# Kernel optimization log

Measured on AMD Instinct MI355X. Metric: run time of the kernel, lower is better.

## Reference

```python
import jax, jax.numpy as jnp
import numpy as np

N = 8192
INPUT_DIM = 256
HIDDEN_DIM = 16
K_NEIGHBORS = 6


def setup_inputs() -> dict:
    key = jax.random.key(0)
    k1, k2 = jax.random.split(key)
    x = jax.random.normal(k1, (N, INPUT_DIM), dtype=jnp.float32)
    W = jax.random.normal(k2, (HIDDEN_DIM, INPUT_DIM), dtype=jnp.float32) * (1.0 / np.sqrt(INPUT_DIM))
    b = jnp.zeros((HIDDEN_DIM,), dtype=jnp.float32)
    return {"x": x, "W": W, "b": b}


def reference(x, W, b):
    num_nodes = x.shape[0]
    # Linear projection then L2-normalize rows (F.normalize, p=2, dim=1, eps=1e-12)
    h = x @ W.T + b                                   # [N, H]
    norm = jnp.linalg.norm(h, axis=1, keepdims=True)
    h = h / jnp.maximum(norm, 1e-12)
    sim = h @ h.T                                     # [N, N] cosine similarity
    k = min(K_NEIGHBORS, num_nodes - 1)
    # top-(k+1) per row; drop the first (self, sim=1 is the max)
    top_vals, top_idx = jax.lax.top_k(sim, k + 1)     # [N, k+1]
    neigh_idx = top_idx[:, 1:]                        # [N, k]
    neigh_vals = top_vals[:, 1:]                      # [N, k]
    rows = jnp.arange(num_nodes)[:, None]             # [N, 1]
    adj = jnp.zeros_like(sim).at[rows, neigh_idx].set(neigh_vals)
    adj = (adj + adj.T) * 0.5
    row_sums = adj.sum(axis=1, keepdims=True)
    adj = adj / (row_sums + 1e-8)
    return adj
```

## Files before the change

kernel.cpp:

```cpp
#include <hip/hip_runtime.h>
#include <stdint.h>
#include <math.h>

#define NN   8192
#define IND  256
#define HID  16
#define KN   6
#define SEG  8
#define SW   (NN/SEG)
#define CCOL 256
#define NCH  (SW/CCOL)
#define TPC  (CCOL/16)


typedef short s8v  __attribute__((ext_vector_type(8)));
typedef float f4v  __attribute__((ext_vector_type(4)));

__device__ __forceinline__ uint32_t fflip(float f) {
    const uint32_t u = __float_as_uint(f);
    return (u & 0x80000000u) ? ~u : (u | 0x80000000u);
}

__device__ __forceinline__ uint32_t bf16_rne_bits(float x) {
    const uint32_t u = __float_as_uint(x);
    return (u + 0x7FFFu + ((u >> 16) & 1u)) & 0xFFFF0000u;
}

__global__ __launch_bounds__(256) void k1_embed(const float* __restrict__ x,
                                                const float* __restrict__ W,
                                                const float* __restrict__ b,
                                                ushort* __restrict__ PA1,
                                                ushort* __restrict__ PA2,
                                                ushort* __restrict__ PA3,
                                                ushort* __restrict__ PB1,
                                                ushort* __restrict__ PB2,
                                                float* __restrict__ rs,
                                                int* __restrict__ cnt)
{
    const int lane = threadIdx.x & 63;
    const int wv   = threadIdx.x >> 6;
    const int row  = blockIdx.x * 4 + wv;

    const float4 xv = *(const float4*)(x + (size_t)row * IND + lane * 4);

    float hv[HID];
#pragma unroll
    for (int k = 0; k < HID; ++k) {
        const float4 wv4 = *(const float4*)(W + (size_t)k * IND + lane * 4);
        float v = xv.x * wv4.x + xv.y * wv4.y + xv.z * wv4.z + xv.w * wv4.w;
#pragma unroll
        for (int m = 32; m >= 1; m >>= 1) v += __shfl_xor(v, m, 64);
        hv[k] = v;
    }

    float ss = 0.f;
#pragma unroll
    for (int k = 0; k < HID; ++k) { hv[k] = hv[k] + b[k]; ss += hv[k] * hv[k]; }
    const float nrm = fmaxf(sqrtf(ss), 1e-12f);
#pragma unroll
    for (int k = 0; k < HID; ++k) hv[k] = hv[k] / nrm;

    if (lane == 0) { rs[row] = 0.f; cnt[row] = 0; }

    if (lane < 32) {
        const int s = lane, k = s & 15;
        const float xx = hv[k];
        const uint32_t hb = bf16_rne_bits(xx);
        const float r1 = xx - __uint_as_float(hb);
        const uint32_t mb = bf16_rne_bits(r1);
        const float r2 = r1 - __uint_as_float(mb);
        const uint32_t lb = bf16_rne_bits(r2);
        const ushort hi = (ushort)(hb >> 16);
        const ushort mi = (ushort)(mb >> 16);
        const ushort lo = (ushort)(lb >> 16);

        const bool f = (s < 16);
        const size_t t = (size_t)row * 32 + s;
        PA1[t] = hi;
        PA2[t] = f ? mi : hi;
        PA3[t] = f ? lo : mi;
        PB1[t] = f ? hi : mi;
        PB2[t] = f ? hi : lo;
    }
}

#define CSWPF(X,i,j) { const float _h = fmaxf(X[i], X[j]); const float _l = fminf(X[i], X[j]); X[i] = _h; X[j] = _l; }
#define CSWPV(a,b)   { const float _h = fmaxf(a, b); const float _l = fminf(a, b); a = _h; b = _l; }
#define BSTAGES(X) CSWPF(X,0,4) CSWPF(X,1,5) CSWPF(X,2,6) CSWPF(X,3,7) \
                   CSWPF(X,0,2) CSWPF(X,1,3) CSWPF(X,4,6) CSWPF(X,5,7) \
                   CSWPF(X,0,1) CSWPF(X,2,3) CSWPF(X,4,5) CSWPF(X,6,7)

__global__ __launch_bounds__(256, 4) void p1_scan(const ushort* __restrict__ PA1,
                                                  const ushort* __restrict__ PA2,
                                                  const ushort* __restrict__ PA3,
                                                  const ushort* __restrict__ PB1,
                                                  const ushort* __restrict__ PB2,
                                                  float* __restrict__ tq)
{
    __shared__ s8v lds[2048];

    const int tid  = threadIdx.x;
    const int lane = tid & 63;
    const int wv   = tid >> 6;
    const int seg  = blockIdx.x & (SEG - 1);
    const int row0 = (blockIdx.x >> 3) * 64 + wv * 16;
    const int n    = lane & 15;
    const int q    = lane >> 4;
    const int qs   = (q + ((n >> 1) & 3)) & 3;

    const size_t ioff = ((size_t)(row0 + n) << 5) + (q << 3);
    const s8v i1 = *(const s8v*)(PA1 + ioff);
    const s8v i2 = *(const s8v*)(PA2 + ioff);
    const s8v i3 = *(const s8v*)(PA3 + ioff);

    float L[8];
#pragma unroll
    for (int t = 0; t < 8; ++t) L[t] = -INFINITY;

    for (int cc = 0; cc < NCH; ++cc) {
        __syncthreads();
#pragma unroll
        for (int it = 0; it < 8; ++it) {
            const int o  = it * 256 + tid;
            const int oo = o & 1023;
            const int c  = oo >> 2;
            const int qq = oo & 3;
            const int sw = (qq + ((c >> 1) & 3)) & 3;
            const ushort* src = (it < 4) ? PB1 : PB2;
            const int gcol = seg * SW + cc * CCOL + c;
            const s8v v = *(const s8v*)(src + ((size_t)gcol << 5) + (qq << 3));
            lds[((it < 4) ? 0 : 1024) + (c << 2) + sw] = v;
        }
        __syncthreads();

        const int base = (n << 2) + qs;
#pragma unroll 4
        for (int t = 0; t < TPC; ++t) {
            const s8v jb1 = lds[t * 64 + base];
            const s8v jb2 = lds[1024 + t * 64 + base];

            f4v acc = {0.f, 0.f, 0.f, 0.f};
            acc = __builtin_amdgcn_mfma_f32_16x16x32_bf16(jb1, i1, acc, 0, 0, 0);
            acc = __builtin_amdgcn_mfma_f32_16x16x32_bf16(jb2, i2, acc, 0, 0, 0);
            acc = __builtin_amdgcn_mfma_f32_16x16x32_bf16(jb1, i3, acc, 0, 0, 0);

            float s0 = acc[0], s1 = acc[1], s2 = acc[2], s3 = acc[3];
            CSWPV(s0, s1) CSWPV(s2, s3) CSWPV(s0, s2) CSWPV(s1, s3) CSWPV(s1, s2)

            L[4] = fmaxf(L[4], s3);
            L[5] = fmaxf(L[5], s2);
            L[6] = fmaxf(L[6], s1);
            L[7] = fmaxf(L[7], s0);
            BSTAGES(L)
        }
    }

#pragma unroll
    for (int mm = 16; mm <= 32; mm <<= 1) {
        float o[8], X[8];
#pragma unroll
        for (int t = 0; t < 8; ++t) o[t] = __shfl_xor(L[t], mm, 64);
#pragma unroll
        for (int t = 0; t < 8; ++t) X[t] = fmaxf(L[t], o[7 - t]);
        BSTAGES(X)
#pragma unroll
        for (int t = 0; t < 8; ++t) L[t] = X[t];
    }

    if (q == 0) {
        float* dst = tq + ((size_t)seg * NN + (row0 + n)) * 8;
#pragma unroll
        for (int t = 0; t < 8; ++t) dst[t] = L[t];
    }
}

__global__ __launch_bounds__(256, 4) void p2_emit(const ushort* __restrict__ PA1,
                                                  const ushort* __restrict__ PA2,
                                                  const ushort* __restrict__ PA3,
                                                  const ushort* __restrict__ PB1,
                                                  const ushort* __restrict__ PB2,
                                                  const float* __restrict__ tq,
                                                  int* __restrict__ cnt,
                                                  float* __restrict__ candv,
                                                  int* __restrict__ candj)
{
    __shared__ s8v lds[2048];
    __shared__ float tau_s[64];

    const int tid  = threadIdx.x;
    const int lane = tid & 63;
    const int wv   = tid >> 6;
    const int seg  = blockIdx.x & (SEG - 1);
    const int rg0  = (blockIdx.x >> 3) * 64;
    const int row0 = rg0 + wv * 16;
    const int n    = lane & 15;
    const int q    = lane >> 4;
    const int qs   = (q + ((n >> 1) & 3)) & 3;
    const int row  = row0 + n;

    if (tid < 64) {
        const int r = rg0 + tid;
        float hd[SEG]; int ix[SEG];
#pragma unroll
        for (int s = 0; s < SEG; ++s) { hd[s] = tq[((size_t)s * NN + r) * 8]; ix[s] = 0; }
        float tv0 = -INFINITY;
#pragma unroll
        for (int t = 0; t < 8; ++t) {
            float best = hd[0]; int bs = 0;
#pragma unroll
            for (int s = 1; s < SEG; ++s)
                if (hd[s] > best) { best = hd[s]; bs = s; }
            tv0 = best;
            ++ix[bs];
            hd[bs] = (ix[bs] < 8) ? tq[((size_t)bs * NN + r) * 8 + ix[bs]] : -INFINITY;
        }
        tau_s[tid] = tv0;
    }
    __syncthreads();
    const float tv = tau_s[wv * 16 + n];

    const size_t ioff = ((size_t)row << 5) + (q << 3);
    const s8v i1 = *(const s8v*)(PA1 + ioff);
    const s8v i2 = *(const s8v*)(PA2 + ioff);
    const s8v i3 = *(const s8v*)(PA3 + ioff);

    for (int cc = 0; cc < NCH; ++cc) {
        __syncthreads();
#pragma unroll
        for (int it = 0; it < 8; ++it) {
            const int o  = it * 256 + tid;
            const int oo = o & 1023;
            const int c  = oo >> 2;
            const int qq = oo & 3;
            const int sw = (qq + ((c >> 1) & 3)) & 3;
            const ushort* src = (it < 4) ? PB1 : PB2;
            const int gcol = seg * SW + cc * CCOL + c;
            const s8v v = *(const s8v*)(src + ((size_t)gcol << 5) + (qq << 3));
            lds[((it < 4) ? 0 : 1024) + (c << 2) + sw] = v;
        }
        __syncthreads();

        const int base = (n << 2) + qs;
#pragma unroll 4
        for (int t = 0; t < TPC; ++t) {
            const s8v jb1 = lds[t * 64 + base];
            const s8v jb2 = lds[1024 + t * 64 + base];

            f4v acc = {0.f, 0.f, 0.f, 0.f};
            acc = __builtin_amdgcn_mfma_f32_16x16x32_bf16(jb1, i1, acc, 0, 0, 0);
            acc = __builtin_amdgcn_mfma_f32_16x16x32_bf16(jb2, i2, acc, 0, 0, 0);
            acc = __builtin_amdgcn_mfma_f32_16x16x32_bf16(jb1, i3, acc, 0, 0, 0);

            const float vm = fmaxf(fmaxf(acc[0], acc[1]), fmaxf(acc[2], acc[3]));
            if (__builtin_expect(vm >= tv, 0)) {
                const int jbase = seg * SW + cc * CCOL + t * 16 + (q << 2);
#pragma unroll
                for (int g = 0; g < 4; ++g) {
                    if (acc[g] >= tv) {
                        const int idx = atomicAdd(&cnt[row], 1);
                        if (idx < 16) {
                            candv[(size_t)row * 16 + idx] = acc[g];
                            candj[(size_t)row * 16 + idx] = jbase + g;
                        }
                    }
                }
            }
        }
    }
}

__global__ __launch_bounds__(256) void p3_select(const int* __restrict__ cnt,
                                                 const float* __restrict__ candv,
                                                 const int* __restrict__ candj,
                                                 int* __restrict__ nbr_idx,
                                                 float* __restrict__ nbr_val,
                                                 float* __restrict__ rs)
{
    const int row = blockIdx.x * 256 + threadIdx.x;
    const int c = min(cnt[row], 16);
    uint64_t keys[16];
    for (int i = 0; i < c; ++i) {
        const float v = candv[(size_t)row * 16 + i];
        const uint32_t j = (uint32_t)candj[(size_t)row * 16 + i];
        keys[i] = ((uint64_t)fflip(v) << 32) | (uint64_t)(~j);
    }
    for (int t = 0; t < 7; ++t) {
        uint64_t best = 0; int bi = 0;
        for (int i = 0; i < c; ++i)
            if (keys[i] > best) { best = keys[i]; bi = i; }
        keys[bi] = 0;
        if (t >= 1) {
            uint32_t u = (uint32_t)(best >> 32);
            u = (u & 0x80000000u) ? (u & 0x7fffffffu) : ~u;
            const float v = __uint_as_float(u);
            const int j = (int)~(uint32_t)best;
            nbr_val[(size_t)row * KN + (t - 1)] = v;
            nbr_idx[(size_t)row * KN + (t - 1)] = j;
            atomicAdd(&rs[row], v * 0.5f);
            atomicAdd(&rs[j],   v * 0.5f);
        }
    }
}

__global__ __launch_bounds__(256) void k5_scatter(const int* __restrict__ nbr_idx,
                                                  const float* __restrict__ nbr_val,
                                                  const float* __restrict__ rs,
                                                  float* __restrict__ out)
{
    const int e = blockIdx.x * 256 + threadIdx.x;
    const int i = e / KN;
    const int j = nbr_idx[e];
    const float v = nbr_val[e] * 0.5f;
    const float wi = v / (rs[i] + 1e-8f);
    const float wj = v / (rs[j] + 1e-8f);
    atomicAdd(out + (size_t)i * NN + j, wi);
    atomicAdd(out + (size_t)j * NN + i, wj);
}

extern "C" void kernel_launch(void* const* d_in, const int* in_sizes, int n_in,
                              void* d_out, int out_size, void* d_ws, size_t ws_size,
                              hipStream_t stream)
{
    const float* x = (const float*)d_in[0];
    const float* W = (const float*)d_in[1];
    const float* b = (const float*)d_in[2];
    float* out = (float*)d_out;

    float* tq    = (float*)d_ws;
    float* rs    = tq + (size_t)SEG * NN * 8;
    float* nv    = rs + NN;
    float* candv = nv + (size_t)NN * KN;
    int*   ni    = (int*)(candv + (size_t)NN * 16);
    int*   candj = ni + (size_t)NN * KN;
    int*   cnt   = candj + (size_t)NN * 16;
    ushort* PA1  = (ushort*)(cnt + NN);
    ushort* PA2  = PA1 + (size_t)NN * 32;
    ushort* PA3  = PA2 + (size_t)NN * 32;
    ushort* PB1  = PA3 + (size_t)NN * 32;
    ushort* PB2  = PB1 + (size_t)NN * 32;

    k1_embed <<<NN / 4,            256, 0, stream>>>(x, W, b, PA1, PA2, PA3, PB1, PB2, rs, cnt);
    p1_scan  <<<(NN / 64) * SEG,   256, 0, stream>>>(PA1, PA2, PA3, PB1, PB2, tq);
    p2_emit  <<<(NN / 64) * SEG,   256, 0, stream>>>(PA1, PA2, PA3, PB1, PB2, tq, cnt, candv, candj);
    p3_select<<<NN / 256,          256, 0, stream>>>(cnt, candv, candj, ni, nv, rs);
    k5_scatter<<<(NN * KN) / 256,  256, 0, stream>>>(ni, nv, rs, out);
}
```

Baseline: 328.9 us.

## Track per-lane top-3 instead of top-8 in scan pass, widen candidate buffer

In the first scan pass each lane now keeps only its top 3 similarity values with a small min/max merge network, instead of a full bitonic top-8 list updated every tile. The per-tile sort and merge work in the hot loop shrinks. The per-row threshold is still the 8th largest, built by merging across lanes, but from fewer candidates per lane, so it is looser. That lets more candidates through in the emit pass, so the candidate buffer grows from 16 to 32 entries per row to avoid overflow. The costs are more atomics and candidate writes in the emit pass, a larger selection array in the select pass, and a risk of dropping true neighbours if more than 32 values pass the threshold.

Measured after the change: 333.1 us (median of 2 runs). Within noise of the previous version (+1.3%).

```diff
diff --git a/kernel.cpp b/kernel.cpp
--- a/kernel.cpp
+++ b/kernel.cpp
@@ -11,6 +11,7 @@
 #define CCOL 256
 #define NCH  (SW/CCOL)
 #define TPC  (CCOL/16)
+#define CCAP 32
 
 
 typedef short s8v  __attribute__((ext_vector_type(8)));
@@ -113,9 +114,7 @@
     const s8v i2 = *(const s8v*)(PA2 + ioff);
     const s8v i3 = *(const s8v*)(PA3 + ioff);
 
-    float L[8];
-#pragma unroll
-    for (int t = 0; t < 8; ++t) L[t] = -INFINITY;
+    float L0 = -INFINITY, L1 = -INFINITY, L2 = -INFINITY;
 
     for (int cc = 0; cc < NCH; ++cc) {
         __syncthreads();
@@ -144,33 +143,45 @@
             acc = __builtin_amdgcn_mfma_f32_16x16x32_bf16(jb2, i2, acc, 0, 0, 0);
             acc = __builtin_amdgcn_mfma_f32_16x16x32_bf16(jb1, i3, acc, 0, 0, 0);
 
-            float s0 = acc[0], s1 = acc[1], s2 = acc[2], s3 = acc[3];
-            CSWPV(s0, s1) CSWPV(s2, s3) CSWPV(s0, s2) CSWPV(s1, s3) CSWPV(s1, s2)
-
-            L[4] = fmaxf(L[4], s3);
-            L[5] = fmaxf(L[5], s2);
-            L[6] = fmaxf(L[6], s1);
-            L[7] = fmaxf(L[7], s0);
-            BSTAGES(L)
-        }
-    }
-
-#pragma unroll
-    for (int mm = 16; mm <= 32; mm <<= 1) {
+            float a0 = acc[0], a1 = acc[1], a2 = acc[2], a3 = acc[3];
+            CSWPV(a0, a1) CSWPV(a2, a3) CSWPV(a0, a2)
+            const float s1 = fmaxf(fmaxf(a1, a2), a3);
+            const float s2 = fmaxf(fminf(a1, a2),
+                                   fminf(fmaxf(a1, a2), a3));
+
+            const float n0 = fmaxf(L0, a0);
+            const float n1 = fmaxf(fmaxf(L1, s1), fminf(L0, a0));
+            const float n2 = fmaxf(fmaxf(L2, s2),
+                                   fmaxf(fminf(L0, s1), fminf(L1, a0)));
+            L0 = n0; L1 = n1; L2 = n2;
+        }
+    }
+
+    float R[8];
+    {
+        float P[4] = {L0, L1, L2, -INFINITY};
+        float o[4];
+#pragma unroll
+        for (int t = 0; t < 4; ++t) o[t] = __shfl_xor(P[t], 16, 64);
+        R[0] = P[0]; R[1] = P[1]; R[2] = P[2]; R[3] = P[3];
+        R[4] = o[3]; R[5] = o[2]; R[6] = o[1]; R[7] = o[0];
+        BSTAGES(R)
+    }
+    {
         float o[8], X[8];
 #pragma unroll
-        for (int t = 0; t < 8; ++t) o[t] = __shfl_xor(L[t], mm, 64);
-#pragma unroll
-        for (int t = 0; t < 8; ++t) X[t] = fmaxf(L[t], o[7 - t]);
+        for (int t = 0; t < 8; ++t) o[t] = __shfl_xor(R[t], 32, 64);
+#pragma unroll
+        for (int t = 0; t < 8; ++t) X[t] = fmaxf(R[t], o[7 - t]);
         BSTAGES(X)
 #pragma unroll
-        for (int t = 0; t < 8; ++t) L[t] = X[t];
+        for (int t = 0; t < 8; ++t) R[t] = X[t];
     }
 
     if (q == 0) {
         float* dst = tq + ((size_t)seg * NN + (row0 + n)) * 8;
 #pragma unroll
-        for (int t = 0; t < 8; ++t) dst[t] = L[t];
+        for (int t = 0; t < 8; ++t) dst[t] = R[t];
     }
 }
 
@@ -258,9 +269,9 @@
                 for (int g = 0; g < 4; ++g) {
                     if (acc[g] >= tv) {
                         const int idx = atomicAdd(&cnt[row], 1);
-                        if (idx < 16) {
-                            candv[(size_t)row * 16 + idx] = acc[g];
-                            candj[(size_t)row * 16 + idx] = jbase + g;
+                        if (idx < CCAP) {
+                            candv[(size_t)row * CCAP + idx] = acc[g];
+                            candj[(size_t)row * CCAP + idx] = jbase + g;
                         }
                     }
                 }
@@ -277,11 +288,11 @@
                                                  float* __restrict__ rs)
 {
     const int row = blockIdx.x * 256 + threadIdx.x;
-    const int c = min(cnt[row], 16);
-    uint64_t keys[16];
+    const int c = min(cnt[row], CCAP);
+    uint64_t keys[CCAP];
     for (int i = 0; i < c; ++i) {
-        const float v = candv[(size_t)row * 16 + i];
-        const uint32_t j = (uint32_t)candj[(size_t)row * 16 + i];
+        const float v = candv[(size_t)row * CCAP + i];
+        const uint32_t j = (uint32_t)candj[(size_t)row * CCAP + i];
         keys[i] = ((uint64_t)fflip(v) << 32) | (uint64_t)(~j);
     }
     for (int t = 0; t < 7; ++t) {
@@ -330,9 +341,9 @@
     float* rs    = tq + (size_t)SEG * NN * 8;
     float* nv    = rs + NN;
     float* candv = nv + (size_t)NN * KN;
-    int*   ni    = (int*)(candv + (size_t)NN * 16);
+    int*   ni    = (int*)(candv + (size_t)NN * CCAP);
     int*   candj = ni + (size_t)NN * KN;
-    int*   cnt   = candj + (size_t)NN * 16;
+    int*   cnt   = candj + (size_t)NN * CCAP;
     ushort* PA1  = (ushort*)(cnt + NN);
     ushort* PA2  = PA1 + (size_t)NN * 32;
     ushort* PA3  = PA2 + (size_t)NN * 32;
```
